# Kernel optimization log

Measured on AMD Instinct MI355X. Metric: run time of the kernel, lower is better.

Reference implementation:

```python
import jax, jax.numpy as jnp
import numpy as np


def setup_inputs() -> dict:
    key = jax.random.key(0)
    k1, k2, k3, k4, k5 = jax.random.split(key, 5)
    B, C, T, N = 32, 1024, 1024, 3
    video = jax.random.normal(k1, (B, C, T, 1, 1), dtype=jnp.float32)
    length = jax.random.randint(k2, (B,), 1, T + 1).astype(jnp.int32)
    center = 0.5 * jax.random.normal(k3, (N,), dtype=jnp.float32)
    delta = 0.01 * jax.random.normal(k4, (N,), dtype=jnp.float32)
    gamma = 0.0001 * jax.random.normal(k5, (N,), dtype=jnp.float32)
    return {"video": video, "length": length, "center": center,
            "delta": delta, "gamma": gamma}


def reference(video, length, center, delta, gamma):
    B, C, T = video.shape[0], video.shape[1], video.shape[2]
    N = center.shape[0]
    v = video.reshape(B, C, T)
    c = jnp.tanh(center)                                  # (N,)
    g = jnp.tanh(gamma)                                   # (N,)
    lf = length.astype(jnp.float32)                       # (B,)
    # per-(batch, filter) Cauchy center; delta is multiplied by zeros in the
    # original code and therefore has no effect on the output.
    centers = (lf[:, None] - 1.0) * (c[None, :] + 1.0) / 2.0   # (B, N)
    gammas = jnp.exp(1.5 - 2.0 * jnp.abs(g))              # (N,)
    t = jnp.arange(T, dtype=jnp.float32)                  # (T,)
    diff = (t[None, None, :] - centers[:, :, None]) / gammas[None, :, None]
    f = 1.0 / (jnp.pi * gammas[None, :, None] * (1.0 + diff * diff))  # (B,N,T)
    f = f / (jnp.sum(f, axis=2, keepdims=True) + 1e-6)
    # pooled output: for each batch/channel, N weighted time-averages
    o = jnp.einsum('bnt,bct->bcn', f, v)                  # (B, C, N)
    return o.reshape(B, C * N)
```

## Files before the change

kernel.cpp:

```cpp
#include <hip/hip_runtime.h>
#include <math.h>

constexpr int B = 32;
constexpr int C = 1024;
constexpr int T = 1024;
constexpr int N = 3;
constexpr int CPB = 16;

__global__ __launch_bounds__(256) void tsf_fused(
    const float* __restrict__ v ,
    const int* __restrict__ length,
    const float* __restrict__ center,
    const float* __restrict__ gamma_,
    float* __restrict__ out ) {
  const int groups_per_b = C / CPB;
  const int b = blockIdx.x / groups_per_b;
  const int cg = blockIdx.x % groups_per_b;

  __shared__ float fs[N][T];
  __shared__ float wsum[N][4];

  const int lane = threadIdx.x & 63;
  const int wv = threadIdx.x >> 6;

  const float lf = (float)length[b];

  float vals[N][4];
#pragma unroll
  for (int n = 0; n < N; ++n) {
    const float c = tanhf(center[n]);
    const float g = tanhf(gamma_[n]);
    const float ctr = (lf - 1.0f) * (c + 1.0f) * 0.5f;
    const float gam = expf(1.5f - 2.0f * fabsf(g));
    const float inv_gam = 1.0f / gam;
    const float pref = 1.0f / (3.14159265358979f * gam);

    float s = 0.0f;
#pragma unroll
    for (int i = 0; i < 4; ++i) {
      const float t = (float)(threadIdx.x + i * 256);
      const float d = (t - ctr) * inv_gam;
      vals[n][i] = pref / (1.0f + d * d);
      s += vals[n][i];
    }
#pragma unroll
    for (int off = 32; off > 0; off >>= 1) s += __shfl_down(s, off);
    if (lane == 0) wsum[n][wv] = s;
  }
  __syncthreads();

#pragma unroll
  for (int n = 0; n < N; ++n) {
    const float inv =
        1.0f / (wsum[n][0] + wsum[n][1] + wsum[n][2] + wsum[n][3] + 1e-6f);
#pragma unroll
    for (int i = 0; i < 4; ++i)
      fs[n][threadIdx.x + i * 256] = vals[n][i] * inv;
  }
  __syncthreads();

  const float4* w0 = (const float4*)(&fs[0][0]);
  const float4* w1 = (const float4*)(&fs[1][0]);
  const float4* w2 = (const float4*)(&fs[2][0]);

  for (int cc = wv; cc < CPB; cc += 4) {
    const int ch = cg * CPB + cc;
    const float4* row = (const float4*)(v + ((size_t)b * C + ch) * T);

    float a0 = 0.f, a1 = 0.f, a2 = 0.f;
#pragma unroll
    for (int i = lane; i < T / 4; i += 64) {
      const float4 x = row[i];
      const float4 q0 = w0[i];
      const float4 q1 = w1[i];
      const float4 q2 = w2[i];
      a0 += x.x * q0.x + x.y * q0.y + x.z * q0.z + x.w * q0.w;
      a1 += x.x * q1.x + x.y * q1.y + x.z * q1.z + x.w * q1.w;
      a2 += x.x * q2.x + x.y * q2.y + x.z * q2.z + x.w * q2.w;
    }

#pragma unroll
    for (int off = 32; off > 0; off >>= 1) {
      a0 += __shfl_down(a0, off);
      a1 += __shfl_down(a1, off);
      a2 += __shfl_down(a2, off);
    }

    if (lane == 0) {
      float* o = out + ((size_t)b * C + ch) * N;
      o[0] = a0;
      o[1] = a1;
      o[2] = a2;
    }
  }
}

extern "C" void kernel_launch(void* const* d_in, const int* in_sizes, int n_in,
                              void* d_out, int out_size, void* d_ws,
                              size_t ws_size, hipStream_t stream) {
  const float* video = (const float*)d_in[0];
  const int* length = (const int*)d_in[1];
  const float* center = (const float*)d_in[2];
  const float* gamma_ = (const float*)d_in[4];
  float* out = (float*)d_out;

  tsf_fused<<<B * (C / CPB), 256, 0, stream>>>(video, length, center, gamma_,
                                               out);
}
```

Before: 30.00 us.

## Keep Cauchy weights in registers and prefetch video rows before compute

```diff
diff --git a/kernel.cpp b/kernel.cpp
--- a/kernel.cpp
+++ b/kernel.cpp
@@ -6,6 +6,17 @@
 constexpr int T = 1024;
 constexpr int N = 3;
 constexpr int CPB = 16;
+constexpr int CPW = 4;
+
+__device__ __forceinline__ float wred(float x) {
+#pragma unroll
+  for (int off = 32; off > 0; off >>= 1) x += __shfl_down(x, off);
+  return x;
+}
+
+__device__ __forceinline__ float dot4(const float4 a, const float4 b) {
+  return a.x * b.x + a.y * b.y + a.z * b.z + a.w * b.w;
+}
 
 __global__ __launch_bounds__(256) void tsf_fused(
     const float* __restrict__ v ,
@@ -16,81 +27,95 @@
   const int groups_per_b = C / CPB;
   const int b = blockIdx.x / groups_per_b;
   const int cg = blockIdx.x % groups_per_b;
-
-  __shared__ float fs[N][T];
-  __shared__ float wsum[N][4];
-
   const int lane = threadIdx.x & 63;
   const int wv = threadIdx.x >> 6;
+  const int ch0 = cg * CPB + wv * CPW;
+
+  const float4* row0 = (const float4*)(v + ((size_t)b * C + ch0 + 0) * T);
+  const float4* row1 = (const float4*)(v + ((size_t)b * C + ch0 + 1) * T);
+  const float4* row2 = (const float4*)(v + ((size_t)b * C + ch0 + 2) * T);
+  const float4* row3 = (const float4*)(v + ((size_t)b * C + ch0 + 3) * T);
+
+  float4 xa0 = row0[lane];
+  float4 xa1 = row0[lane + 64];
+  float4 xa2 = row0[lane + 128];
+  float4 xa3 = row0[lane + 192];
+  float4 xb0 = row1[lane];
+  float4 xb1 = row1[lane + 64];
+  float4 xb2 = row1[lane + 128];
+  float4 xb3 = row1[lane + 192];
 
   const float lf = (float)length[b];
-
-  float vals[N][4];
+  float4 w[N][4];
+  float s[N];
+  float pref[N];
 #pragma unroll
   for (int n = 0; n < N; ++n) {
     const float c = tanhf(center[n]);
     const float g = tanhf(gamma_[n]);
     const float ctr = (lf - 1.0f) * (c + 1.0f) * 0.5f;
     const float gam = expf(1.5f - 2.0f * fabsf(g));
-    const float inv_gam = 1.0f / gam;
-    const float pref = 1.0f / (3.14159265358979f * gam);
+    const float a = 1.0f / gam;
+    const float bb = -ctr * a;
+    pref[n] = 1.0f / (3.14159265358979f * gam);
+    s[n] = 0.0f;
+#pragma unroll
+    for (int k = 0; k < 4; ++k) {
+      const float t0 = (float)(4 * lane + 256 * k);
+      float4 wk;
+      float d;
+      d = fmaf(t0 + 0.0f, a, bb); wk.x = 1.0f / fmaf(d, d, 1.0f);
+      d = fmaf(t0 + 1.0f, a, bb); wk.y = 1.0f / fmaf(d, d, 1.0f);
+      d = fmaf(t0 + 2.0f, a, bb); wk.z = 1.0f / fmaf(d, d, 1.0f);
+      d = fmaf(t0 + 3.0f, a, bb); wk.w = 1.0f / fmaf(d, d, 1.0f);
+      w[n][k] = wk;
+      s[n] += (wk.x + wk.y) + (wk.z + wk.w);
+    }
+  }
 
-    float s = 0.0f;
-#pragma unroll
-    for (int i = 0; i < 4; ++i) {
-      const float t = (float)(threadIdx.x + i * 256);
-      const float d = (t - ctr) * inv_gam;
-      vals[n][i] = pref / (1.0f + d * d);
-      s += vals[n][i];
-    }
-#pragma unroll
-    for (int off = 32; off > 0; off >>= 1) s += __shfl_down(s, off);
-    if (lane == 0) wsum[n][wv] = s;
-  }
-  __syncthreads();
+  float acc[CPW][N];
 
 #pragma unroll
-  for (int n = 0; n < N; ++n) {
-    const float inv =
-        1.0f / (wsum[n][0] + wsum[n][1] + wsum[n][2] + wsum[n][3] + 1e-6f);
-#pragma unroll
-    for (int i = 0; i < 4; ++i)
-      fs[n][threadIdx.x + i * 256] = vals[n][i] * inv;
-  }
-  __syncthreads();
-
-  const float4* w0 = (const float4*)(&fs[0][0]);
-  const float4* w1 = (const float4*)(&fs[1][0]);
-  const float4* w2 = (const float4*)(&fs[2][0]);
-
-  for (int cc = wv; cc < CPB; cc += 4) {
-    const int ch = cg * CPB + cc;
-    const float4* row = (const float4*)(v + ((size_t)b * C + ch) * T);
-
-    float a0 = 0.f, a1 = 0.f, a2 = 0.f;
-#pragma unroll
-    for (int i = lane; i < T / 4; i += 64) {
-      const float4 x = row[i];
-      const float4 q0 = w0[i];
-      const float4 q1 = w1[i];
-      const float4 q2 = w2[i];
-      a0 += x.x * q0.x + x.y * q0.y + x.z * q0.z + x.w * q0.w;
-      a1 += x.x * q1.x + x.y * q1.y + x.z * q1.z + x.w * q1.w;
-      a2 += x.x * q2.x + x.y * q2.y + x.z * q2.z + x.w * q2.w;
-    }
+  for (int n = 0; n < N; ++n)
+    acc[0][n] = dot4(xa0, w[n][0]) + dot4(xa1, w[n][1]) +
+                dot4(xa2, w[n][2]) + dot4(xa3, w[n][3]);
+  xa0 = row2[lane];
+  xa1 = row2[lane + 64];
+  xa2 = row2[lane + 128];
+  xa3 = row2[lane + 192];
 
 #pragma unroll
-    for (int off = 32; off > 0; off >>= 1) {
-      a0 += __shfl_down(a0, off);
-      a1 += __shfl_down(a1, off);
-      a2 += __shfl_down(a2, off);
-    }
+  for (int n = 0; n < N; ++n)
+    acc[1][n] = dot4(xb0, w[n][0]) + dot4(xb1, w[n][1]) +
+                dot4(xb2, w[n][2]) + dot4(xb3, w[n][3]);
+  xb0 = row3[lane];
+  xb1 = row3[lane + 64];
+  xb2 = row3[lane + 128];
+  xb3 = row3[lane + 192];
 
-    if (lane == 0) {
-      float* o = out + ((size_t)b * C + ch) * N;
-      o[0] = a0;
-      o[1] = a1;
-      o[2] = a2;
+#pragma unroll
+  for (int n = 0; n < N; ++n)
+    acc[2][n] = dot4(xa0, w[n][0]) + dot4(xa1, w[n][1]) +
+                dot4(xa2, w[n][2]) + dot4(xa3, w[n][3]);
+#pragma unroll
+  for (int n = 0; n < N; ++n)
+    acc[3][n] = dot4(xb0, w[n][0]) + dot4(xb1, w[n][1]) +
+                dot4(xb2, w[n][2]) + dot4(xb3, w[n][3]);
+
+#pragma unroll
+  for (int cc = 0; cc < CPW; ++cc)
+#pragma unroll
+    for (int n = 0; n < N; ++n) acc[cc][n] = wred(acc[cc][n]);
+#pragma unroll
+  for (int n = 0; n < N; ++n) s[n] = wred(s[n]);
+
+  if (lane == 0) {
+#pragma unroll
+    for (int n = 0; n < N; ++n) {
+      const float scale = pref[n] / fmaf(pref[n], s[n], 1e-6f);
+#pragma unroll
+      for (int cc = 0; cc < CPW; ++cc)
+        out[((size_t)b * C + ch0 + cc) * N + n] = acc[cc][n] * scale;
     }
   }
 }
```

New measurement: 30.98 us. +3.3%, slower.

## Prefetch first video row before filter setup and defer normalization to outputs

Applied to the files above, without the earlier changes.

```diff
diff --git a/kernel.cpp b/kernel.cpp
--- a/kernel.cpp
+++ b/kernel.cpp
@@ -6,6 +6,18 @@
 constexpr int T = 1024;
 constexpr int N = 3;
 constexpr int CPB = 16;
+constexpr int CPW = 4;
+
+typedef float f4 __attribute__((ext_vector_type(4)));
+
+__device__ __forceinline__ float dot4(const f4 a, const f4 b) {
+  return a.x * b.x + a.y * b.y + a.z * b.z + a.w * b.w;
+}
+
+__device__ __forceinline__ float fast_tanh(float x) {
+  const float e = __expf(2.0f * x);
+  return 1.0f - 2.0f / (e + 1.0f);
+}
 
 __global__ __launch_bounds__(256) void tsf_fused(
     const float* __restrict__ v ,
@@ -13,70 +25,92 @@
     const float* __restrict__ center,
     const float* __restrict__ gamma_,
     float* __restrict__ out ) {
-  const int groups_per_b = C / CPB;
-  const int b = blockIdx.x / groups_per_b;
-  const int cg = blockIdx.x % groups_per_b;
-
-  __shared__ float fs[N][T];
-  __shared__ float wsum[N][4];
-
+  const int b = blockIdx.x >> 6;
+  const int cg = blockIdx.x & 63;
   const int lane = threadIdx.x & 63;
   const int wv = threadIdx.x >> 6;
 
+  __shared__ float fs[N][T];
+  __shared__ float wsumS[N][4];
+
+  const int ch0 = cg * CPB + wv * CPW;
+  const f4* r0 = (const f4*)(v + ((size_t)b * C + ch0) * T);
+
+  f4 x0 = r0[lane];
+  f4 x1 = r0[lane + 64];
+
   const float lf = (float)length[b];
-
-  float vals[N][4];
+  float scale[N];
 #pragma unroll
   for (int n = 0; n < N; ++n) {
-    const float c = tanhf(center[n]);
-    const float g = tanhf(gamma_[n]);
+    const float c = fast_tanh(center[n]);
+    const float g = fast_tanh(gamma_[n]);
     const float ctr = (lf - 1.0f) * (c + 1.0f) * 0.5f;
-    const float gam = expf(1.5f - 2.0f * fabsf(g));
+    const float gam = __expf(1.5f - 2.0f * fabsf(g));
     const float inv_gam = 1.0f / gam;
-    const float pref = 1.0f / (3.14159265358979f * gam);
+    scale[n] = 1.0f / (3.14159265358979f * gam);
 
     float s = 0.0f;
 #pragma unroll
     for (int i = 0; i < 4; ++i) {
       const float t = (float)(threadIdx.x + i * 256);
       const float d = (t - ctr) * inv_gam;
-      vals[n][i] = pref / (1.0f + d * d);
-      s += vals[n][i];
+      const float u = 1.0f / fmaf(d, d, 1.0f);
+      fs[n][threadIdx.x + i * 256] = u;
+      s += u;
     }
 #pragma unroll
     for (int off = 32; off > 0; off >>= 1) s += __shfl_down(s, off);
-    if (lane == 0) wsum[n][wv] = s;
+    if (lane == 0) wsumS[n][wv] = s;
   }
   __syncthreads();
 
 #pragma unroll
   for (int n = 0; n < N; ++n) {
-    const float inv =
-        1.0f / (wsum[n][0] + wsum[n][1] + wsum[n][2] + wsum[n][3] + 1e-6f);
+    const float s = wsumS[n][0] + wsumS[n][1] + wsumS[n][2] + wsumS[n][3];
+    scale[n] = scale[n] / fmaf(scale[n], s, 1e-6f);
+  }
+
+  const f4* w0 = (const f4*)(&fs[0][0]);
+  const f4* w1 = (const f4*)(&fs[1][0]);
+  const f4* w2 = (const f4*)(&fs[2][0]);
+
+  {
+    const f4 x2 = r0[lane + 128];
+    const f4 x3 = r0[lane + 192];
+
+    float a0 = dot4(x0, w0[lane]) + dot4(x1, w0[lane + 64]) +
+               dot4(x2, w0[lane + 128]) + dot4(x3, w0[lane + 192]);
+    float a1 = dot4(x0, w1[lane]) + dot4(x1, w1[lane + 64]) +
+               dot4(x2, w1[lane + 128]) + dot4(x3, w1[lane + 192]);
+    float a2 = dot4(x0, w2[lane]) + dot4(x1, w2[lane + 64]) +
+               dot4(x2, w2[lane + 128]) + dot4(x3, w2[lane + 192]);
+
 #pragma unroll
-    for (int i = 0; i < 4; ++i)
-      fs[n][threadIdx.x + i * 256] = vals[n][i] * inv;
+    for (int off = 32; off > 0; off >>= 1) {
+      a0 += __shfl_down(a0, off);
+      a1 += __shfl_down(a1, off);
+      a2 += __shfl_down(a2, off);
+    }
+    if (lane == 0) {
+      float* o = out + ((size_t)b * C + ch0) * N;
+      o[0] = a0 * scale[0];
+      o[1] = a1 * scale[1];
+      o[2] = a2 * scale[2];
+    }
   }
-  __syncthreads();
 
-  const float4* w0 = (const float4*)(&fs[0][0]);
-  const float4* w1 = (const float4*)(&fs[1][0]);
-  const float4* w2 = (const float4*)(&fs[2][0]);
-
-  for (int cc = wv; cc < CPB; cc += 4) {
-    const int ch = cg * CPB + cc;
-    const float4* row = (const float4*)(v + ((size_t)b * C + ch) * T);
+  for (int cc = 1; cc < CPW; ++cc) {
+    const int ch = ch0 + cc;
+    const f4* row = (const f4*)(v + ((size_t)b * C + ch) * T);
 
     float a0 = 0.f, a1 = 0.f, a2 = 0.f;
 #pragma unroll
     for (int i = lane; i < T / 4; i += 64) {
-      const float4 x = row[i];
-      const float4 q0 = w0[i];
-      const float4 q1 = w1[i];
-      const float4 q2 = w2[i];
-      a0 += x.x * q0.x + x.y * q0.y + x.z * q0.z + x.w * q0.w;
-      a1 += x.x * q1.x + x.y * q1.y + x.z * q1.z + x.w * q1.w;
-      a2 += x.x * q2.x + x.y * q2.y + x.z * q2.z + x.w * q2.w;
+      const f4 x = row[i];
+      a0 += dot4(x, w0[i]);
+      a1 += dot4(x, w1[i]);
+      a2 += dot4(x, w2[i]);
     }
 
 #pragma unroll
@@ -88,9 +122,9 @@
 
     if (lane == 0) {
       float* o = out + ((size_t)b * C + ch) * N;
-      o[0] = a0;
-      o[1] = a1;
-      o[2] = a2;
+      o[0] = a0 * scale[0];
+      o[1] = a1 * scale[1];
+      o[2] = a2 * scale[2];
     }
   }
 }
```

After: 28.88 us. 1.04x faster.
